# Optimization experiments

Hardware: AMD Instinct MI355X
Metric: run time of the kernel (lower is better)

Reference implementation:

```python
import jax, jax.numpy as jnp
import numpy as np

# CrossAttention (DFFNet): 1x1 convs produce q,k from depth and v from rgb;
# full dense attention over hw spatial tokens: softmax(q^T k) then v @ mask^T.

def setup_inputs() -> dict:
    key = jax.random.key(0)
    ks = jax.random.split(key, 8)
    B, C, H, W = 4, 256, 64, 64
    Cqk = C // 8  # ratio=8 -> 32
    s = 0.02
    return {
        "rgb":   jax.random.normal(ks[0], (B, C, H, W), jnp.float32),
        "depth": jax.random.normal(ks[1], (B, C, H, W), jnp.float32),
        "Wq": jax.random.normal(ks[2], (Cqk, C), jnp.float32) * s,
        "bq": jax.random.normal(ks[3], (Cqk,), jnp.float32) * s,
        "Wk": jax.random.normal(ks[4], (Cqk, C), jnp.float32) * s,
        "bk": jax.random.normal(ks[5], (Cqk,), jnp.float32) * s,
        "Wv": jax.random.normal(ks[6], (C, C), jnp.float32) * s,
        "bv": jax.random.normal(ks[7], (C,), jnp.float32) * s,
    }


def reference(rgb, depth, Wq, bq, Wk, bk, Wv, bv):
    B, C, H, W = rgb.shape
    hw = H * W
    d = depth.reshape(B, C, hw)   # [B, C, hw]
    r = rgb.reshape(B, C, hw)     # [B, C, hw]
    # 1x1 convs == channel-mixing linear maps
    q = jnp.einsum('oc,bcn->bon', Wq, d) + bq[None, :, None]  # [B, Cqk, hw]
    k = jnp.einsum('oc,bcn->bon', Wk, d) + bk[None, :, None]  # [B, Cqk, hw]
    v = jnp.einsum('oc,bcn->bon', Wv, r) + bv[None, :, None]  # [B, C, hw]
    # scores: q^T k -> [B, hw, hw], softmax over last dim
    scores = jnp.einsum('bcn,bcm->bnm', q, k)
    mask = jax.nn.softmax(scores, axis=-1)
    # feat = v @ mask^T  -> [B, C, hw]
    feat = jnp.einsum('bcm,bnm->bcn', v, mask)
    return feat.reshape(B, C, H, W)
```

## Files before the change

kernel.cpp:

```cpp
#include <hip/hip_runtime.h>
#include <stdint.h>

#define L2E 1.44269504088896340736f

typedef _Float16 half8 __attribute__((ext_vector_type(8)));
typedef float floatx4 __attribute__((ext_vector_type(4)));

static __device__ __forceinline__ unsigned short f32_to_f16u(float f) {
  union { _Float16 h; unsigned short s; } cv; cv.h = (_Float16)f; return cv.s;
}

static __device__ __forceinline__ float fast_exp2(float x) {
  float r;
  asm("v_exp_f32 %0, %1" : "=v"(r) : "v"(x));
  return r;
}

__global__ __launch_bounds__(256) void proj_kernel(
    const float* __restrict__ rgb,
    const float* __restrict__ depth,
    const float* __restrict__ Wq, const float* __restrict__ bq,
    const float* __restrict__ Wk, const float* __restrict__ bk,
    const float* __restrict__ Wv, const float* __restrict__ bv,
    unsigned short* __restrict__ qT,
    unsigned short* __restrict__ kT,
    unsigned short* __restrict__ v)
{
  __shared__ __align__(16) unsigned short sW[64 * 256];

  const int n0 = blockIdx.x * 64;
  const int b  = blockIdx.y;
  const int z  = blockIdx.z;
  const int t  = threadIdx.x;
  const int w  = t >> 6;
  const int lane = t & 63;
  const int l15 = lane & 15;
  const int q4  = lane >> 4;

  const float* X = (z == 0) ? depth : rgb;
  const float* xb = X + (size_t)b * 256 * 4096;
  const int n_row = n0 + 16 * w + l15;

  half8 a8[8];
#pragma unroll
  for (int ks = 0; ks < 8; ks++) {
#pragma unroll
    for (int j = 0; j < 8; j++) {
      int c = ks * 32 + q4 * 8 + j;
      a8[ks][j] = (_Float16)xb[(size_t)c * 4096 + n_row];
    }
  }

  const int nq = (z == 0) ? 1 : 2;
  for (int qd = 0; qd < nq; qd++) {
    const int colbase = (z == 0) ? 0 : (z - 1) * 128 + qd * 64;
    __syncthreads();

#pragma unroll
    for (int it = 0; it < 8; it++) {
      int L = it * 256 + t;
      int og = L >> 5;
      int phys = L & 31;
      int ci = phys ^ (og & 7);
      const float* wr;
      if (z == 0) wr = (og < 32) ? (Wq + (size_t)og * 256) : (Wk + (size_t)(og - 32) * 256);
      else        wr = Wv + (size_t)(colbase + og) * 256;
      float4 w0 = *(const float4*)(wr + ci * 8);
      float4 w1 = *(const float4*)(wr + ci * 8 + 4);
      half8 h;
      h[0] = (_Float16)w0.x; h[1] = (_Float16)w0.y; h[2] = (_Float16)w0.z; h[3] = (_Float16)w0.w;
      h[4] = (_Float16)w1.x; h[5] = (_Float16)w1.y; h[6] = (_Float16)w1.z; h[7] = (_Float16)w1.w;
      *(half8*)&sW[(size_t)L * 8] = h;
    }

    float bias[4];
#pragma unroll
    for (int ct = 0; ct < 4; ct++) {
      int og = ct * 16 + l15;
      if (z == 0) bias[ct] = (og < 32) ? bq[og] : bk[og - 32];
      else        bias[ct] = bv[colbase + og];
    }
    __syncthreads();

    floatx4 acc[4];
#pragma unroll
    for (int i = 0; i < 4; i++) acc[i] = (floatx4){0.f, 0.f, 0.f, 0.f};

#pragma unroll
    for (int ks = 0; ks < 8; ks++) {
      const int ci = ks * 4 + q4;
#pragma unroll
      for (int ct = 0; ct < 4; ct++) {
        int og = ct * 16 + l15;
        half8 bf = *(const half8*)&sW[og * 256 + ((ci ^ (og & 7)) * 8)];
        acc[ct] = __builtin_amdgcn_mfma_f32_16x16x32_f16(a8[ks], bf, acc[ct], 0, 0, 0);
      }
    }

    __syncthreads();

    if (z == 0) {
#pragma unroll
      for (int ct = 0; ct < 4; ct++) {
        int og = ct * 16 + l15;
#pragma unroll
        for (int r = 0; r < 4; r++) {
          int n = n0 + 16 * w + q4 * 4 + r;
          unsigned short hv = f32_to_f16u(acc[ct][r] + bias[ct]);
          if (og < 32) qT[((size_t)b * 4096 + n) * 32 + og] = hv;
          else         kT[((size_t)b * 4096 + n) * 32 + (og - 32)] = hv;
        }
      }
    } else {
      unsigned short* tile = sW;
#pragma unroll
      for (int ct = 0; ct < 4; ct++) {
#pragma unroll
        for (int r = 0; r < 4; r++) {
          int co_l = ct * 16 + l15;
          int nl = 16 * w + q4 * 4 + r;
          tile[co_l * 72 + nl] = f32_to_f16u(acc[ct][r] + bias[ct]);
        }
      }
      __syncthreads();
#pragma unroll
      for (int it = 0; it < 2; it++) {
        int co_l = it * 32 + (t >> 3);
        int ch = t & 7;
        int4 val = *(const int4*)&tile[co_l * 72 + ch * 8];
        *(int4*)&v[((size_t)b * 256 + colbase + co_l) * 4096 + n0 + ch * 8] = val;
      }
    }
  }
}

__global__ __launch_bounds__(256, 3) void attn_kernel(
    const unsigned short* __restrict__ qT,
    const unsigned short* __restrict__ kT,
    const unsigned short* __restrict__ v,
    unsigned short* __restrict__ Op,
    float* __restrict__ lW)
{
  __shared__ __align__(16) unsigned char smem[18432];
  unsigned short* sP = (unsigned short*)smem;

  const int n0 = blockIdx.x * 64;
  const int b  = blockIdx.y;
  const int chunk = blockIdx.z;
  const int t  = threadIdx.x;
  const int w  = t >> 6;
  const int lane = t & 63;
  const int l15 = lane & 15;
  const int q4  = lane >> 4;

  half8 aq = *(const half8*)(qT + ((size_t)b * 4096 + n0 + 16 * w + l15) * 32 + q4 * 8);

  const unsigned short* kL = kT + (size_t)b * 4096 * 32 + (size_t)l15 * 32 + q4 * 8;
  const unsigned short* vL = v + ((size_t)b * 256 + w * 64 + l15) * 4096 + q4 * 8;

  float lsum[4] = {0.f, 0.f, 0.f, 0.f};
  floatx4 acc[16];
#pragma unroll
  for (int ct = 0; ct < 16; ct++) acc[ct] = (floatx4){0.f, 0.f, 0.f, 0.f};
  const floatx4 zf = (floatx4){0.f, 0.f, 0.f, 0.f};

  const int mbase = chunk * 1024;

  half8 kc0 = *(const half8*)(kL + (size_t)mbase * 32);
  half8 kc1 = *(const half8*)(kL + (size_t)(mbase + 16) * 32);
  half8 vc0 = *(const half8*)(vL + mbase);
  half8 vc1 = *(const half8*)(vL + 65536 + mbase);
  half8 vc2 = *(const half8*)(vL + 131072 + mbase);
  half8 vc3 = *(const half8*)(vL + 196608 + mbase);

  unsigned short* sPw = sP + w * 640;

  for (int it = 0; it < 32; ++it) {
    const int m0 = mbase + it * 32;
    const int bufo = (it & 1) * 2560;
    half8 kn0 = kc0, kn1 = kc1, vn0 = vc0, vn1 = vc1, vn2 = vc2, vn3 = vc3;
    if (it < 31) {
      kn0 = *(const half8*)(kL + (size_t)(m0 + 32) * 32);
      kn1 = *(const half8*)(kL + (size_t)(m0 + 48) * 32);
      vn0 = *(const half8*)(vL + m0 + 32);
      vn1 = *(const half8*)(vL + 65536 + m0 + 32);
      vn2 = *(const half8*)(vL + 131072 + m0 + 32);
      vn3 = *(const half8*)(vL + 196608 + m0 + 32);
    }

    floatx4 s0 = __builtin_amdgcn_mfma_f32_16x16x32_f16(aq, kc0, zf, 0, 0, 0);
    floatx4 s1 = __builtin_amdgcn_mfma_f32_16x16x32_f16(aq, kc1, zf, 0, 0, 0);

    float p0[4], p1[4];
#pragma unroll
    for (int r = 0; r < 4; r++) {
      p0[r] = fast_exp2(s0[r] * L2E);
      p1[r] = fast_exp2(s1[r] * L2E);
      lsum[r] += p0[r] + p1[r];
    }
#pragma unroll
    for (int r = 0; r < 4; r++) {
      int row = q4 * 4 + r;
      sPw[bufo + row * 40 + l15]      = f32_to_f16u(p0[r]);
      sPw[bufo + row * 40 + 16 + l15] = f32_to_f16u(p1[r]);
    }
    asm volatile("s_waitcnt lgkmcnt(0)" ::: "memory");
    __builtin_amdgcn_s_barrier();
    asm volatile("" ::: "memory");

    half8 ap[4];
#pragma unroll
    for (int nt = 0; nt < 4; nt++)
      ap[nt] = *(const half8*)&sP[bufo + nt * 640 + l15 * 40 + q4 * 8];

#pragma unroll
    for (int ct = 0; ct < 4; ct++) {
      half8 bv8 = (ct == 0) ? vc0 : (ct == 1) ? vc1 : (ct == 2) ? vc2 : vc3;
#pragma unroll
      for (int nt = 0; nt < 4; nt++)
        acc[ct * 4 + nt] = __builtin_amdgcn_mfma_f32_16x16x32_f16(ap[nt], bv8, acc[ct * 4 + nt], 0, 0, 0);
    }

    kc0 = kn0; kc1 = kn1; vc0 = vn0; vc1 = vn1; vc2 = vn2; vc3 = vn3;
  }

#pragma unroll
  for (int off = 1; off < 16; off <<= 1) {
#pragma unroll
    for (int r = 0; r < 4; r++) lsum[r] += __shfl_xor(lsum[r], off);
  }
  if (l15 == 0) {
#pragma unroll
    for (int r = 0; r < 4; r++)
      lW[((size_t)chunk * 4 + b) * 4096 + n0 + 16 * w + q4 * 4 + r] = lsum[r];
  }

  unsigned short* sO = (unsigned short*)smem;
#pragma unroll
  for (int pass = 0; pass < 2; pass++) {
    __syncthreads();
    if ((w >> 1) == pass) {
#pragma unroll
      for (int ct = 0; ct < 4; ct++) {
        int co_l = (w & 1) * 64 + ct * 16 + l15;
#pragma unroll
        for (int nt = 0; nt < 4; nt++) {
#pragma unroll
          for (int r = 0; r < 4; r++) {
            int nl = nt * 16 + q4 * 4 + r;
            sO[co_l * 72 + nl] = f32_to_f16u(acc[ct * 4 + nt][r]);
          }
        }
      }
    }
    __syncthreads();
#pragma unroll
    for (int s = 0; s < 4; s++) {
      int co_l = s * 32 + (t >> 3);
      int ch = t & 7;
      int4 val = *(const int4*)&sO[co_l * 72 + ch * 8];
      *(int4*)&Op[(((size_t)chunk * 4 + b) * 256 + pass * 128 + co_l) * 4096 + n0 + ch * 8] = val;
    }
  }
}

__global__ __launch_bounds__(256) void combine_kernel(
    const unsigned short* __restrict__ Op,
    const float* __restrict__ lW,
    float* __restrict__ out)
{
  const int t = threadIdx.x;
  const int b = blockIdx.y;
  const size_t n8 = (size_t)blockIdx.x * 2048 + (size_t)t * 8;
  const int co0 = blockIdx.z * 8;

  float sum[8] = {0.f, 0.f, 0.f, 0.f, 0.f, 0.f, 0.f, 0.f};
#pragma unroll
  for (int ch = 0; ch < 4; ch++) {
    const float* lp = lW + ((size_t)ch * 4 + b) * 4096 + n8;
    float4 a0 = *(const float4*)lp;
    float4 a1 = *(const float4*)(lp + 4);
    sum[0] += a0.x; sum[1] += a0.y; sum[2] += a0.z; sum[3] += a0.w;
    sum[4] += a1.x; sum[5] += a1.y; sum[6] += a1.z; sum[7] += a1.w;
  }
  float rl[8];
#pragma unroll
  for (int i = 0; i < 8; i++) rl[i] = 1.0f / sum[i];

#pragma unroll
  for (int cc = 0; cc < 8; cc++) {
    int co = co0 + cc;
    float o[8] = {0.f, 0.f, 0.f, 0.f, 0.f, 0.f, 0.f, 0.f};
#pragma unroll
    for (int ch = 0; ch < 4; ch++) {
      half8 hv = *(const half8*)&Op[(((size_t)ch * 4 + b) * 256 + co) * 4096 + n8];
#pragma unroll
      for (int i = 0; i < 8; i++) o[i] += (float)hv[i];
    }
    float* op = out + ((size_t)b * 256 + co) * 4096 + n8;
    float4 r0, r1;
    r0.x = o[0] * rl[0]; r0.y = o[1] * rl[1]; r0.z = o[2] * rl[2]; r0.w = o[3] * rl[3];
    r1.x = o[4] * rl[4]; r1.y = o[5] * rl[5]; r1.z = o[6] * rl[6]; r1.w = o[7] * rl[7];
    *(float4*)op = r0;
    *(float4*)(op + 4) = r1;
  }
}

extern "C" void kernel_launch(void* const* d_in, const int* in_sizes, int n_in,
                              void* d_out, int out_size, void* d_ws, size_t ws_size,
                              hipStream_t stream) {
  const float* rgb   = (const float*)d_in[0];
  const float* depth = (const float*)d_in[1];
  const float* Wq    = (const float*)d_in[2];
  const float* bq    = (const float*)d_in[3];
  const float* Wk    = (const float*)d_in[4];
  const float* bk    = (const float*)d_in[5];
  const float* Wv    = (const float*)d_in[6];
  const float* bv    = (const float*)d_in[7];
  float* out = (float*)d_out;

  unsigned short* qT = (unsigned short*)d_ws;
  unsigned short* kT = qT + (size_t)4 * 4096 * 32;
  unsigned short* vW = kT + (size_t)4 * 4096 * 32;
  unsigned short* Op = vW + (size_t)4 * 256 * 4096;
  float* lW = (float*)(Op + (size_t)4 * 4 * 256 * 4096);

  dim3 pg(64, 4, 3);
  proj_kernel<<<pg, 256, 0, stream>>>(rgb, depth, Wq, bq, Wk, bk, Wv, bv, qT, kT, vW);
  dim3 ag(64, 4, 4);
  attn_kernel<<<ag, 256, 0, stream>>>(qT, kT, vW, Op, lW);
  dim3 cg(2, 4, 32);
  combine_kernel<<<cg, 256, 0, stream>>>(Op, lW, out);
}
```

Before: 180.8 us.

## Stage V via async global-to-LDS loads, coalesce projection input, retile combine

The attention kernel now streams V tiles into swizzled, double-buffered LDS with global_load_lds, replacing per-lane register loads, and manually unrolls by two with explicit vmcnt waits. Occupancy is raised to 4 blocks per CU despite the larger shared-memory footprint. The projection kernel loads its input tile into LDS with coalesced float4 reads before building MFMA fragments, and processes weights in 32-column slices. The combine kernel halves the channels per block to launch twice as many blocks. Together these target uncoalesced global loads and latency, at the cost of more LDS traffic and hand-tuned wait counts that could race if the counts are wrong.

```diff
diff --git a/kernel.cpp b/kernel.cpp
--- a/kernel.cpp
+++ b/kernel.cpp
@@ -14,6 +14,13 @@
   float r;
   asm("v_exp_f32 %0, %1" : "=v"(r) : "v"(x));
   return r;
+}
+
+typedef __attribute__((address_space(3))) unsigned int as3_uint;
+typedef __attribute__((address_space(1))) const unsigned int as1_cuint;
+
+static __device__ __forceinline__ void async16(const void* g, void* l) {
+  __builtin_amdgcn_global_load_lds((as1_cuint*)g, (as3_uint*)l, 16, 0, 0);
 }
 
 __global__ __launch_bounds__(256) void proj_kernel(
@@ -26,7 +33,8 @@
     unsigned short* __restrict__ kT,
     unsigned short* __restrict__ v)
 {
-  __shared__ __align__(16) unsigned short sW[64 * 256];
+  __shared__ __align__(16) unsigned short sX[256 * 76];
+  __shared__ __align__(16) unsigned short sW[32 * 256];
 
   const int n0 = blockIdx.x * 64;
   const int b  = blockIdx.y;
@@ -38,32 +46,44 @@
   const int q4  = lane >> 4;
 
   const float* X = (z == 0) ? depth : rgb;
-  const float* xb = X + (size_t)b * 256 * 4096;
-  const int n_row = n0 + 16 * w + l15;
+  const float* xb = X + (size_t)b * 256 * 4096 + n0;
+
+#pragma unroll
+  for (int i = 0; i < 8; i++) {
+    int h = i * 256 + t;
+    int c = h >> 3, oct = h & 7;
+    const float* src = xb + (size_t)c * 4096 + oct * 8;
+    float4 x0 = *(const float4*)src;
+    float4 x1 = *(const float4*)(src + 4);
+    half8 hh;
+    hh[0] = (_Float16)x0.x; hh[1] = (_Float16)x0.y; hh[2] = (_Float16)x0.z; hh[3] = (_Float16)x0.w;
+    hh[4] = (_Float16)x1.x; hh[5] = (_Float16)x1.y; hh[6] = (_Float16)x1.z; hh[7] = (_Float16)x1.w;
+    *(half8*)&sX[c * 76 + oct * 8] = hh;
+  }
+  __syncthreads();
 
   half8 a8[8];
 #pragma unroll
   for (int ks = 0; ks < 8; ks++) {
 #pragma unroll
     for (int j = 0; j < 8; j++) {
-      int c = ks * 32 + q4 * 8 + j;
-      a8[ks][j] = (_Float16)xb[(size_t)c * 4096 + n_row];
-    }
-  }
-
-  const int nq = (z == 0) ? 1 : 2;
-  for (int qd = 0; qd < nq; qd++) {
-    const int colbase = (z == 0) ? 0 : (z - 1) * 128 + qd * 64;
-    __syncthreads();
-
-#pragma unroll
-    for (int it = 0; it < 8; it++) {
-      int L = it * 256 + t;
+      a8[ks][j] = *(const _Float16*)&sX[(ks * 32 + q4 * 8 + j) * 76 + 16 * w + l15];
+    }
+  }
+
+  const int ns = (z == 0) ? 2 : 4;
+  for (int s = 0; s < ns; s++) {
+    const int colbase = (z == 0) ? 0 : (z - 1) * 128 + s * 32;
+    __syncthreads();
+
+#pragma unroll
+    for (int i = 0; i < 4; i++) {
+      int L = i * 256 + t;
       int og = L >> 5;
       int phys = L & 31;
       int ci = phys ^ (og & 7);
       const float* wr;
-      if (z == 0) wr = (og < 32) ? (Wq + (size_t)og * 256) : (Wk + (size_t)(og - 32) * 256);
+      if (z == 0) wr = ((s == 0) ? Wq : Wk) + (size_t)og * 256;
       else        wr = Wv + (size_t)(colbase + og) * 256;
       float4 w0 = *(const float4*)(wr + ci * 8);
       float4 w1 = *(const float4*)(wr + ci * 8 + 4);
@@ -73,27 +93,27 @@
       *(half8*)&sW[(size_t)L * 8] = h;
     }
 
-    float bias[4];
-#pragma unroll
-    for (int ct = 0; ct < 4; ct++) {
+    float bias2[2];
+#pragma unroll
+    for (int ct = 0; ct < 2; ct++) {
       int og = ct * 16 + l15;
-      if (z == 0) bias[ct] = (og < 32) ? bq[og] : bk[og - 32];
-      else        bias[ct] = bv[colbase + og];
-    }
-    __syncthreads();
-
-    floatx4 acc[4];
-#pragma unroll
-    for (int i = 0; i < 4; i++) acc[i] = (floatx4){0.f, 0.f, 0.f, 0.f};
+      if (z == 0) bias2[ct] = (s == 0) ? bq[og] : bk[og];
+      else        bias2[ct] = bv[colbase + og];
+    }
+    __syncthreads();
+
+    floatx4 acc2[2];
+    acc2[0] = (floatx4){0.f, 0.f, 0.f, 0.f};
+    acc2[1] = (floatx4){0.f, 0.f, 0.f, 0.f};
 
 #pragma unroll
     for (int ks = 0; ks < 8; ks++) {
       const int ci = ks * 4 + q4;
 #pragma unroll
-      for (int ct = 0; ct < 4; ct++) {
+      for (int ct = 0; ct < 2; ct++) {
         int og = ct * 16 + l15;
         half8 bf = *(const half8*)&sW[og * 256 + ((ci ^ (og & 7)) * 8)];
-        acc[ct] = __builtin_amdgcn_mfma_f32_16x16x32_f16(a8[ks], bf, acc[ct], 0, 0, 0);
+        acc2[ct] = __builtin_amdgcn_mfma_f32_16x16x32_f16(a8[ks], bf, acc2[ct], 0, 0, 0);
       }
     }
 
@@ -101,31 +121,30 @@
 
     if (z == 0) {
 #pragma unroll
-      for (int ct = 0; ct < 4; ct++) {
+      for (int ct = 0; ct < 2; ct++) {
         int og = ct * 16 + l15;
 #pragma unroll
         for (int r = 0; r < 4; r++) {
           int n = n0 + 16 * w + q4 * 4 + r;
-          unsigned short hv = f32_to_f16u(acc[ct][r] + bias[ct]);
-          if (og < 32) qT[((size_t)b * 4096 + n) * 32 + og] = hv;
-          else         kT[((size_t)b * 4096 + n) * 32 + (og - 32)] = hv;
+          unsigned short hv = f32_to_f16u(acc2[ct][r] + bias2[ct]);
+          if (s == 0) qT[((size_t)b * 4096 + n) * 32 + og] = hv;
+          else        kT[((size_t)b * 4096 + n) * 32 + og] = hv;
         }
       }
     } else {
       unsigned short* tile = sW;
 #pragma unroll
-      for (int ct = 0; ct < 4; ct++) {
+      for (int ct = 0; ct < 2; ct++) {
 #pragma unroll
         for (int r = 0; r < 4; r++) {
           int co_l = ct * 16 + l15;
           int nl = 16 * w + q4 * 4 + r;
-          tile[co_l * 72 + nl] = f32_to_f16u(acc[ct][r] + bias[ct]);
+          tile[co_l * 72 + nl] = f32_to_f16u(acc2[ct][r] + bias2[ct]);
         }
       }
       __syncthreads();
-#pragma unroll
-      for (int it = 0; it < 2; it++) {
-        int co_l = it * 32 + (t >> 3);
+      {
+        int co_l = t >> 3;
         int ch = t & 7;
         int4 val = *(const int4*)&tile[co_l * 72 + ch * 8];
         *(int4*)&v[((size_t)b * 256 + colbase + co_l) * 4096 + n0 + ch * 8] = val;
@@ -134,15 +153,28 @@
   }
 }
 
-__global__ __launch_bounds__(256, 3) void attn_kernel(
+static __device__ __forceinline__ void stage_vp(
+    const unsigned short* __restrict__ vB, unsigned char* dst,
+    int m0, int lane, int w)
+{
+#pragma unroll
+  for (int j = 0; j < 4; j++) {
+    int c = w * 64 + j * 16 + (lane >> 2);
+    int p = lane & 3;
+    int lc = p ^ ((c >> 1) & 3);
+    async16(&vB[(size_t)c * 4096 + m0 + lc * 8], dst + j * 1024);
+  }
+}
+
+__global__ __launch_bounds__(256, 4) void attn_kernel(
     const unsigned short* __restrict__ qT,
     const unsigned short* __restrict__ kT,
     const unsigned short* __restrict__ v,
     unsigned short* __restrict__ Op,
     float* __restrict__ lW)
 {
-  __shared__ __align__(16) unsigned char smem[18432];
-  unsigned short* sP = (unsigned short*)smem;
+  __shared__ __align__(16) unsigned char smem[43008];
+  unsigned short* sP = (unsigned short*)(smem + 32768);
 
   const int n0 = blockIdx.x * 64;
   const int b  = blockIdx.y;
@@ -155,8 +187,8 @@
 
   half8 aq = *(const half8*)(qT + ((size_t)b * 4096 + n0 + 16 * w + l15) * 32 + q4 * 8);
 
+  const unsigned short* vB = v + (size_t)b * 256 * 4096;
   const unsigned short* kL = kT + (size_t)b * 4096 * 32 + (size_t)l15 * 32 + q4 * 8;
-  const unsigned short* vL = v + ((size_t)b * 256 + w * 64 + l15) * 4096 + q4 * 8;
 
   float lsum[4] = {0.f, 0.f, 0.f, 0.f};
   floatx4 acc[16];
@@ -166,63 +198,59 @@
 
   const int mbase = chunk * 1024;
 
-  half8 kc0 = *(const half8*)(kL + (size_t)mbase * 32);
-  half8 kc1 = *(const half8*)(kL + (size_t)(mbase + 16) * 32);
-  half8 vc0 = *(const half8*)(vL + mbase);
-  half8 vc1 = *(const half8*)(vL + 65536 + mbase);
-  half8 vc2 = *(const half8*)(vL + 131072 + mbase);
-  half8 vc3 = *(const half8*)(vL + 196608 + mbase);
-
-  unsigned short* sPw = sP + w * 640;
-
-  for (int it = 0; it < 32; ++it) {
-    const int m0 = mbase + it * 32;
-    const int bufo = (it & 1) * 2560;
-    half8 kn0 = kc0, kn1 = kc1, vn0 = vc0, vn1 = vc1, vn2 = vc2, vn3 = vc3;
-    if (it < 31) {
-      kn0 = *(const half8*)(kL + (size_t)(m0 + 32) * 32);
-      kn1 = *(const half8*)(kL + (size_t)(m0 + 48) * 32);
-      vn0 = *(const half8*)(vL + m0 + 32);
-      vn1 = *(const half8*)(vL + 65536 + m0 + 32);
-      vn2 = *(const half8*)(vL + 131072 + m0 + 32);
-      vn3 = *(const half8*)(vL + 196608 + m0 + 32);
-    }
-
-    floatx4 s0 = __builtin_amdgcn_mfma_f32_16x16x32_f16(aq, kc0, zf, 0, 0, 0);
-    floatx4 s1 = __builtin_amdgcn_mfma_f32_16x16x32_f16(aq, kc1, zf, 0, 0, 0);
-
-    float p0[4], p1[4];
-#pragma unroll
-    for (int r = 0; r < 4; r++) {
-      p0[r] = fast_exp2(s0[r] * L2E);
-      p1[r] = fast_exp2(s1[r] * L2E);
-      lsum[r] += p0[r] + p1[r];
-    }
-#pragma unroll
-    for (int r = 0; r < 4; r++) {
-      int row = q4 * 4 + r;
-      sPw[bufo + row * 40 + l15]      = f32_to_f16u(p0[r]);
-      sPw[bufo + row * 40 + 16 + l15] = f32_to_f16u(p1[r]);
-    }
-    asm volatile("s_waitcnt lgkmcnt(0)" ::: "memory");
-    __builtin_amdgcn_s_barrier();
-    asm volatile("" ::: "memory");
-
-    half8 ap[4];
-#pragma unroll
-    for (int nt = 0; nt < 4; nt++)
-      ap[nt] = *(const half8*)&sP[bufo + nt * 640 + l15 * 40 + q4 * 8];
-
-#pragma unroll
-    for (int ct = 0; ct < 4; ct++) {
-      half8 bv8 = (ct == 0) ? vc0 : (ct == 1) ? vc1 : (ct == 2) ? vc2 : vc3;
-#pragma unroll
-      for (int nt = 0; nt < 4; nt++)
-        acc[ct * 4 + nt] = __builtin_amdgcn_mfma_f32_16x16x32_f16(ap[nt], bv8, acc[ct * 4 + nt], 0, 0, 0);
-    }
-
-    kc0 = kn0; kc1 = kn1; vc0 = vn0; vc1 = vn1; vc2 = vn2; vc3 = vn3;
-  }
+  stage_vp(vB, smem + (w << 12), mbase, lane, w);
+  half8 kA0 = *(const half8*)(kL + (size_t)mbase * 32);
+  half8 kA1 = *(const half8*)(kL + (size_t)(mbase + 16) * 32);
+  half8 kB0{}, kB1{};
+
+#define ATTN_BODY(IT_, KC0, KC1, KN0, KN1, PF)                                   \
+  {                                                                              \
+    const int it_ = (IT_);                                                       \
+    const int m0_ = mbase + it_ * 32;                                            \
+    asm volatile("" ::: "memory");                                               \
+    if (PF) {                                                                    \
+      stage_vp(vB, smem + ((((it_ + 1) & 1) << 14) + (w << 12)), m0_ + 32, lane, w); \
+      KN0 = *(const half8*)(kL + (size_t)(m0_ + 32) * 32);                       \
+      KN1 = *(const half8*)(kL + (size_t)(m0_ + 48) * 32);                       \
+      asm volatile("s_waitcnt vmcnt(6)" ::: "memory");                           \
+    } else {                                                                     \
+      asm volatile("s_waitcnt vmcnt(0)" ::: "memory");                           \
+    }                                                                            \
+    floatx4 s0 = __builtin_amdgcn_mfma_f32_16x16x32_f16(aq, KC0, zf, 0, 0, 0);   \
+    floatx4 s1 = __builtin_amdgcn_mfma_f32_16x16x32_f16(aq, KC1, zf, 0, 0, 0);   \
+    float p0[4], p1[4];                                                          \
+    _Pragma("unroll") for (int r = 0; r < 4; r++) {                              \
+      p0[r] = fast_exp2(s0[r] * L2E);                                            \
+      p1[r] = fast_exp2(s1[r] * L2E);                                            \
+      lsum[r] += p0[r] + p1[r];                                                  \
+    }                                                                            \
+    unsigned short* sPw_ = sP + ((it_ & 1) ? 2560 : 0) + w * 640;                \
+    _Pragma("unroll") for (int r = 0; r < 4; r++) {                              \
+      int row = q4 * 4 + r;                                                      \
+      sPw_[row * 40 + l15]      = f32_to_f16u(p0[r]);                            \
+      sPw_[row * 40 + 16 + l15] = f32_to_f16u(p1[r]);                            \
+    }                                                                            \
+    asm volatile("s_waitcnt lgkmcnt(0)" ::: "memory");                           \
+    __builtin_amdgcn_s_barrier();                                                \
+    asm volatile("s_waitcnt lgkmcnt(0)" ::: "memory");                           \
+    const unsigned short* sPb_ = sP + ((it_ & 1) ? 2560 : 0);                    \
+    half8 ap[4];                                                                 \
+    _Pragma("unroll") for (int nt = 0; nt < 4; nt++)                             \
+      ap[nt] = *(const half8*)&sPb_[nt * 640 + l15 * 40 + q4 * 8];               \
+    const unsigned short* sVb_ = (const unsigned short*)(smem + ((it_ & 1) << 14)); \
+    _Pragma("unroll") for (int ct = 0; ct < 4; ct++) {                           \
+      int co = w * 64 + ct * 16 + l15;                                           \
+      half8 bv8 = *(const half8*)&sVb_[co * 32 + ((q4 ^ ((co >> 1) & 3)) * 8)];  \
+      _Pragma("unroll") for (int nt = 0; nt < 4; nt++)                           \
+        acc[ct * 4 + nt] = __builtin_amdgcn_mfma_f32_16x16x32_f16(ap[nt], bv8, acc[ct * 4 + nt], 0, 0, 0); \
+    }                                                                            \
+  }
+
+  for (int it2 = 0; it2 < 16; ++it2) {
+    ATTN_BODY(2 * it2,     kA0, kA1, kB0, kB1, true)
+    ATTN_BODY(2 * it2 + 1, kB0, kB1, kA0, kA1, (it2 < 15))
+  }
+#undef ATTN_BODY
 
 #pragma unroll
   for (int off = 1; off < 16; off <<= 1) {
@@ -272,7 +300,7 @@
   const int t = threadIdx.x;
   const int b = blockIdx.y;
   const size_t n8 = (size_t)blockIdx.x * 2048 + (size_t)t * 8;
-  const int co0 = blockIdx.z * 8;
+  const int co0 = blockIdx.z * 4;
 
   float sum[8] = {0.f, 0.f, 0.f, 0.f, 0.f, 0.f, 0.f, 0.f};
 #pragma unroll
@@ -288,7 +316,7 @@
   for (int i = 0; i < 8; i++) rl[i] = 1.0f / sum[i];
 
 #pragma unroll
-  for (int cc = 0; cc < 8; cc++) {
+  for (int cc = 0; cc < 4; cc++) {
     int co = co0 + cc;
     float o[8] = {0.f, 0.f, 0.f, 0.f, 0.f, 0.f, 0.f, 0.f};
 #pragma unroll
@@ -329,6 +357,6 @@
   proj_kernel<<<pg, 256, 0, stream>>>(rgb, depth, Wq, bq, Wk, bk, Wv, bv, qT, kT, vW);
   dim3 ag(64, 4, 4);
   attn_kernel<<<ag, 256, 0, stream>>>(qT, kT, vW, Op, lW);
-  dim3 cg(2, 4, 32);
+  dim3 cg(2, 4, 64);
   combine_kernel<<<cg, 256, 0, stream>>>(Op, lW, out);
 }
```

Result: faster. 171.5 us (-5.2%).
